# Kernel tuning notes

Hardware: AMD Instinct MI355X
Metric: run time of the kernel (lower is better)

The kernel has to match this reference:

```python
import jax, jax.numpy as jnp
import numpy as np

B, T, C, H = 4, 2048, 1024, 16
HD = C // H

def setup_inputs() -> dict:
    key = jax.random.key(0)
    ks = jax.random.split(key, 9)
    s = 1.0 / np.sqrt(C)
    return {
        'x':  jax.random.normal(ks[0], (B, T, C), jnp.float32),
        'Wq': jax.random.normal(ks[1], (C, C), jnp.float32) * s,
        'bq': jnp.zeros((C,), jnp.float32),
        'Wk': jax.random.normal(ks[2], (C, C), jnp.float32) * s,
        'bk': jnp.zeros((C,), jnp.float32),
        'Wv': jax.random.normal(ks[3], (C, C), jnp.float32) * s,
        'bv': jnp.zeros((C,), jnp.float32),
        'Wo': jax.random.normal(ks[4], (C, C), jnp.float32) * s,
        'bo': jnp.zeros((C,), jnp.float32),
    }

def reference(x, Wq, bq, Wk, bk, Wv, bv, Wo, bo):
    Bx, Tx, Cx = x.shape
    # projections (torch Linear: x @ W.T + b); split heads -> (B,H,T,HD)
    def heads(y):
        return y.reshape(Bx, Tx, H, HD).transpose(0, 2, 1, 3)
    q = heads(x @ Wq.T + bq)
    k = heads(x @ Wk.T + bk)
    v = heads(x @ Wv.T + bv)
    # NOTE: original scales by 1/sqrt(embedding_dim), not head_dim
    scale = 1.0 / jnp.sqrt(jnp.asarray(Cx, x.dtype))
    att = jnp.einsum('bhqd,bhkd->bhqk', q, k) * scale
    mask = jnp.tril(jnp.ones((Tx, Tx), dtype=bool))
    att = jnp.where(mask, att, jnp.asarray(-jnp.inf, att.dtype))
    att = jax.nn.softmax(att, axis=-1)
    y = jnp.einsum('bhqk,bhkd->bhqd', att, v)
    y = y.transpose(0, 2, 1, 3).reshape(Bx, Tx, Cx)
    return y @ Wo.T + bo
```

## Files before the change

### kernel.cpp

```cpp
#include <hip/hip_runtime.h>
#include <hip/hip_bf16.h>
#include <stdint.h>

#define NB 4
#define NT 2048
#define NC 1024
#define NH 16
#define NHD 64
#define NM (NB*NT)

typedef __attribute__((ext_vector_type(8))) __bf16 bf16x8;
typedef __attribute__((ext_vector_type(4))) float floatx4;
typedef __attribute__((ext_vector_type(8))) unsigned short ushortx8;

#define AS1(p) ((const __attribute__((address_space(1))) void*)(p))
#define AS3(p) ((__attribute__((address_space(3))) void*)(p))

__device__ __forceinline__ unsigned short f2bf(float f) {
    union { float f; unsigned int u; } v; v.f = f;
    unsigned int u = v.u;
    return (unsigned short)((u + 0x7FFFu + ((u >> 16) & 1u)) >> 16);
}
__device__ __forceinline__ unsigned int pk2(float lo, float hi) {
    union { float f; unsigned int u; } a, b; a.f = hi; b.f = lo;
    return __builtin_amdgcn_perm(a.u, b.u, 0x07060302u);
}


__global__ void cast_x_tiled(const float* __restrict__ in,
                             unsigned short* __restrict__ out, int ntiles) {
    const int wid  = (blockIdx.x * blockDim.x + threadIdx.x) >> 6;
    const int lane = threadIdx.x & 63;
    if (wid >= ntiles) return;
    const int R = wid >> 5, C = wid & 31;
    const float* src = in + ((size_t)(R*16 + (lane >> 2)))*1024 + C*32 + (lane & 3)*8;
    const floatx4 v0 = *(const floatx4*)src;
    const floatx4 v1 = *(const floatx4*)(src + 4);
    ushortx8 o;
    o[0] = f2bf(v0[0]); o[1] = f2bf(v0[1]); o[2] = f2bf(v0[2]); o[3] = f2bf(v0[3]);
    o[4] = f2bf(v1[0]); o[5] = f2bf(v1[1]); o[6] = f2bf(v1[2]); o[7] = f2bf(v1[3]);
    *(ushortx8*)&out[(size_t)wid*512 + (((lane & 3)*16 + (lane >> 2)))*8] = o;
}

__global__ void cast4_tiled(const float* __restrict__ w0, const float* __restrict__ w1,
                            const float* __restrict__ w2, const float* __restrict__ w3,
                            unsigned short* __restrict__ o0, unsigned short* __restrict__ o1,
                            unsigned short* __restrict__ o2, unsigned short* __restrict__ o3,
                            int ntiles) {
    const int wid  = (blockIdx.x * blockDim.x + threadIdx.x) >> 6;
    const int lane = threadIdx.x & 63;
    if (wid >= ntiles) return;
    const float* in; unsigned short* out;
    switch (blockIdx.y) {
        case 0: in = w0; out = o0; break;
        case 1: in = w1; out = o1; break;
        case 2: in = w2; out = o2; break;
        default: in = w3; out = o3; break;
    }
    const int R = wid >> 5, C = wid & 31;
    const float* src = in + ((size_t)(R*16 + (lane >> 2)))*1024 + C*32 + (lane & 3)*8;
    const floatx4 v0 = *(const floatx4*)src;
    const floatx4 v1 = *(const floatx4*)(src + 4);
    ushortx8 o;
    o[0] = f2bf(v0[0]); o[1] = f2bf(v0[1]); o[2] = f2bf(v0[2]); o[3] = f2bf(v0[3]);
    o[4] = f2bf(v1[0]); o[5] = f2bf(v1[1]); o[6] = f2bf(v1[2]); o[7] = f2bf(v1[3]);
    *(ushortx8*)&out[(size_t)wid*512 + (((lane & 3)*16 + (lane >> 2)))*8] = o;
}

#define TM 128
#define TN 128
#define BK 32

__device__ __forceinline__ void gemm_core(
    const unsigned short* __restrict__ A,
    const unsigned short* __restrict__ W,
    const float* __restrict__ bias,
    void* __restrict__ Out,
    unsigned short* As, unsigned short* Bs,
    int m_base, int n_base, int N_out, int K, int mode, float oscale)
{
    const int tid  = threadIdx.x;
    const int lane = tid & 63;
    const int wv   = tid >> 6;
    const int quad = lane >> 4;
    const int l16  = lane & 15;
    const int wm = (wv >> 1) * 64;
    const int wn = (wv & 1) * 64;

    floatx4 acc[4][4];
    #pragma unroll
    for (int i = 0; i < 4; ++i)
        #pragma unroll
        for (int j = 0; j < 4; ++j)
            acc[i][j] = (floatx4){0.f, 0.f, 0.f, 0.f};

    const int kTiles = K / BK;
    const int kct = K >> 5;

    const unsigned short* At = A + ((size_t)((m_base >> 4) + wv*2) * kct) * 512 + (size_t)lane*8;
    const unsigned short* Wt = W + ((size_t)((n_base >> 4) + wv*2) * kct) * 512 + (size_t)lane*8;
    const size_t rstride = (size_t)kct * 512;

    for (int kt = 0; kt < kTiles; ++kt) {
        __syncthreads();
        #pragma unroll
        for (int i = 0; i < 2; ++i) {
            __builtin_amdgcn_global_load_lds(
                AS1(At + (size_t)kt*512 + i*rstride),
                AS3(&As[(wv*2 + i)*512]), 16, 0, 0);
            __builtin_amdgcn_global_load_lds(
                AS1(Wt + (size_t)kt*512 + i*rstride),
                AS3(&Bs[(wv*2 + i)*512]), 16, 0, 0);
        }
        __syncthreads();

        bf16x8 af[4], bfr[4];
        #pragma unroll
        for (int mi = 0; mi < 4; ++mi)
            af[mi] = *(const bf16x8*)&As[((wv >> 1)*4 + mi)*512 + lane*8];
        #pragma unroll
        for (int ni = 0; ni < 4; ++ni)
            bfr[ni] = *(const bf16x8*)&Bs[((wv & 1)*4 + ni)*512 + lane*8];

        #pragma unroll
        for (int mi = 0; mi < 4; ++mi)
            #pragma unroll
            for (int ni = 0; ni < 4; ++ni)
                acc[mi][ni] = __builtin_amdgcn_mfma_f32_16x16x32_bf16(
                    af[mi], bfr[ni], acc[mi][ni], 0, 0, 0);
    }

    #pragma unroll
    for (int mi = 0; mi < 4; ++mi) {
        #pragma unroll
        for (int ni = 0; ni < 4; ++ni) {
            const int col = n_base + wn + ni*16 + l16;
            const float bv = bias[col & 1023];
            #pragma unroll
            for (int r = 0; r < 4; ++r) {
                const int row = m_base + wm + mi*16 + quad*4 + r;
                const float v = (acc[mi][ni][r] + bv) * oscale;
                if (mode == 0) {
                    ((float*)Out)[(size_t)row * N_out + col] = v;
                } else if (mode == 1) {
                    const int bb = row >> 11, t = row & (NT - 1);
                    const int h  = (col >> 6) & (NH - 1), d = col & 63;
                    const int bh = bb * NH + h;
                    const size_t idx =
                        ((size_t)((bh*128 + (t >> 4))*2 + (d >> 5)))*512
                        + (size_t)((((d >> 3) & 3)*16 + (t & 15))*8 + (d & 7));
                    ((unsigned short*)Out)[idx] = f2bf(v);
                } else {
                    const int bb = row >> 11, t = row & (NT - 1);
                    const int h  = (col >> 6) & (NH - 1), hd = col & 63;
                    const int bh = bb * NH + h;
                    const int tk = t & 31;
                    const int qv = (tk >> 2) & 3;
                    const int jv = (tk & 3) + ((tk >> 4) << 2);
                    const size_t idx =
                        ((size_t)((bh*64 + (t >> 5))*4 + (hd >> 4)))*512
                        + (size_t)((qv*16 + (hd & 15))*8 + jv);
                    ((unsigned short*)Out)[idx] = f2bf(v);
                }
            }
        }
    }
}

#define QSCALE (0.03125f * 1.44269504088896340736f)

__global__ __launch_bounds__(256) void gemm_qkv(
    const unsigned short* __restrict__ A,
    const unsigned short* __restrict__ Wq, const unsigned short* __restrict__ Wk,
    const unsigned short* __restrict__ Wv,
    const float* __restrict__ bq, const float* __restrict__ bk,
    const float* __restrict__ bv,
    unsigned short* __restrict__ Qo, unsigned short* __restrict__ Ko,
    unsigned short* __restrict__ Vo)
{
    __shared__ __align__(16) unsigned short As[TM*BK];
    __shared__ __align__(16) unsigned short Bs[TN*BK];
    const int wi = blockIdx.y >> 3;
    const int n_base = (blockIdx.y & 7) * TN;
    const unsigned short* W; const float* bias; void* Out; int mode; float osc;
    if (wi == 0)      { W = Wq; bias = bq; Out = Qo; mode = 1; osc = QSCALE; }
    else if (wi == 1) { W = Wk; bias = bk; Out = Ko; mode = 1; osc = 1.0f; }
    else              { W = Wv; bias = bv; Out = Vo; mode = 2; osc = 1.0f; }
    gemm_core(A, W, bias, Out, As, Bs, blockIdx.x * TM, n_base, NC, NC, mode, osc);
}

__global__ __launch_bounds__(256) void gemm_out(
    const unsigned short* __restrict__ A,
    const unsigned short* __restrict__ W,
    const float* __restrict__ bias,
    float* __restrict__ Out)
{
    __shared__ __align__(16) unsigned short As[TM*BK];
    __shared__ __align__(16) unsigned short Bs[TN*BK];
    gemm_core(A, W, bias, Out, As, Bs, blockIdx.x * TM, blockIdx.y * TN,
              NC, NC, 0, 1.0f);
}

__device__ __forceinline__ void attn_q32(
    const unsigned short* __restrict__ Qf,
    const unsigned short* __restrict__ Kf,
    const unsigned short* __restrict__ Vf,
    unsigned short* __restrict__ Y,
    int bh, int st, int lane)
{
    const int quad = lane >> 4, l16 = lane & 15;
    const int q0 = st * 32;
    const int b = bh >> 4, h = bh & (NH - 1);

    const size_t qbase = ((size_t)(bh*128 + st*2))*1024 + (size_t)lane*8;
    const bf16x8 qa0 = *(const bf16x8*)&Qf[qbase];
    const bf16x8 qa1 = *(const bf16x8*)&Qf[qbase + 512];
    const bf16x8 qb0 = *(const bf16x8*)&Qf[qbase + 1024];
    const bf16x8 qb1 = *(const bf16x8*)&Qf[qbase + 1536];

    const unsigned short* kp = Kf + (size_t)bh*131072 + (size_t)lane*8;
    const unsigned short* vp = Vf + (size_t)bh*131072 + (size_t)lane*8;

    floatx4 oa[4], ob[4];
    #pragma unroll
    for (int nt = 0; nt < 4; ++nt) {
        oa[nt] = (floatx4){0.f,0.f,0.f,0.f};
        ob[nt] = (floatx4){0.f,0.f,0.f,0.f};
    }
    float la = 0.f, lb = 0.f;

    const int Ffull = q0 >> 6;
    const int ntile = Ffull + 1;

    for (int f = 0; f < ntile; ++f) {
        const int j0 = f * 64;
        const bool diag = (f == Ffull);
        bf16x8 kf[4][2], vf[4][2];
        {
            const unsigned short* kt = kp + (size_t)(j0 >> 4) * 1024;
            #pragma unroll
            for (int ct = 0; ct < 4; ++ct) {
                kf[ct][0] = *(const bf16x8*)&kt[ct*1024];
                kf[ct][1] = *(const bf16x8*)&kt[ct*1024 + 512];
            }
            const unsigned short* vt = vp + (size_t)(j0 >> 5) * 2048;
            #pragma unroll
            for (int nt = 0; nt < 4; ++nt) {
                vf[nt][0] = *(const bf16x8*)&vt[nt*512];
                vf[nt][1] = *(const bf16x8*)&vt[2048 + nt*512];
            }
        }
        #pragma unroll
        for (int sub = 0; sub < 2; ++sub) {
            const bf16x8 qx0 = sub ? qb0 : qa0;
            const bf16x8 qx1 = sub ? qb1 : qa1;
            floatx4* ox = sub ? ob : oa;

            floatx4 s[4];
            __builtin_amdgcn_s_setprio(1);
            #pragma unroll
            for (int ct = 0; ct < 4; ++ct) {
                s[ct] = (floatx4){0.f,0.f,0.f,0.f};
                s[ct] = __builtin_amdgcn_mfma_f32_16x16x32_bf16(kf[ct][0], qx0, s[ct], 0,0,0);
                s[ct] = __builtin_amdgcn_mfma_f32_16x16x32_bf16(kf[ct][1], qx1, s[ct], 0,0,0);
            }
            __builtin_amdgcn_s_setprio(0);
            float p[4][4];
            float lsum = 0.f;
            if (!diag) {
                #pragma unroll
                for (int ct = 0; ct < 4; ++ct)
                    #pragma unroll
                    for (int r = 0; r < 4; ++r) {
                        p[ct][r] = __builtin_amdgcn_exp2f(s[ct][r]);
                        lsum += p[ct][r];
                    }
            } else {
                const int row = q0 + sub*16 + l16;
                #pragma unroll
                for (int ct = 0; ct < 4; ++ct)
                    #pragma unroll
                    for (int r = 0; r < 4; ++r) {
                        const int key = j0 + ct*16 + quad*4 + r;
                        p[ct][r] = (key <= row) ? __builtin_amdgcn_exp2f(s[ct][r]) : 0.f;
                        lsum += p[ct][r];
                    }
            }
            if (sub) lb += lsum; else la += lsum;

            union { bf16x8 v; unsigned int u[4]; } pf0, pf1;
            pf0.u[0] = pk2(p[0][0], p[0][1]); pf0.u[1] = pk2(p[0][2], p[0][3]);
            pf0.u[2] = pk2(p[1][0], p[1][1]); pf0.u[3] = pk2(p[1][2], p[1][3]);
            pf1.u[0] = pk2(p[2][0], p[2][1]); pf1.u[1] = pk2(p[2][2], p[2][3]);
            pf1.u[2] = pk2(p[3][0], p[3][1]); pf1.u[3] = pk2(p[3][2], p[3][3]);

            __builtin_amdgcn_s_setprio(1);
            #pragma unroll
            for (int nt = 0; nt < 4; ++nt) {
                ox[nt] = __builtin_amdgcn_mfma_f32_16x16x32_bf16(vf[nt][0], pf0.v, ox[nt], 0,0,0);
                ox[nt] = __builtin_amdgcn_mfma_f32_16x16x32_bf16(vf[nt][1], pf1.v, ox[nt], 0,0,0);
            }
            __builtin_amdgcn_s_setprio(0);
        }
    }

    la += __shfl_xor(la, 16); la += __shfl_xor(la, 32);
    lb += __shfl_xor(lb, 16); lb += __shfl_xor(lb, 32);
    const float ia = 1.0f / la, ib = 1.0f / lb;

    const size_t Rbase = (size_t)((b*NT + q0) >> 4);
    const int cg = (quad >> 1), co = (quad & 1)*4;
    #pragma unroll
    for (int nt = 0; nt < 4; ++nt) {
        const size_t base = ((Rbase*32 + h*2 + (nt >> 1))*512)
                          + (size_t)((((nt & 1)*2 + cg)*16 + l16)*8 + co);
        ushort4 wa, wb;
        wa.x = f2bf(oa[nt][0]*ia); wa.y = f2bf(oa[nt][1]*ia);
        wa.z = f2bf(oa[nt][2]*ia); wa.w = f2bf(oa[nt][3]*ia);
        wb.x = f2bf(ob[nt][0]*ib); wb.y = f2bf(ob[nt][1]*ib);
        wb.z = f2bf(ob[nt][2]*ib); wb.w = f2bf(ob[nt][3]*ib);
        *(ushort4*)&Y[base]         = wa;
        *(ushort4*)&Y[base + 16384] = wb;
    }
}

__global__ __launch_bounds__(256) void flash_attn(
    const unsigned short* __restrict__ Qf,
    const unsigned short* __restrict__ Kf,
    const unsigned short* __restrict__ Vf,
    unsigned short* __restrict__ Y)
{
    const int tid  = threadIdx.x;
    const int wave = tid >> 6;
    const int lane = tid & 63;
    const int L  = blockIdx.x;
    const int bh = (L & 7) * 8 + ((L >> 3) & 7);
    const int x  = L >> 6;
    const int w  = x * 4 + wave;
    attn_q32(Qf, Kf, Vf, Y, bh, w, lane);
    attn_q32(Qf, Kf, Vf, Y, bh, 63 - w, lane);
}

extern "C" void kernel_launch(void* const* d_in, const int* in_sizes, int n_in,
                              void* d_out, int out_size, void* d_ws, size_t ws_size,
                              hipStream_t stream) {
    const float* x  = (const float*)d_in[0];
    const float* Wq = (const float*)d_in[1];
    const float* bq = (const float*)d_in[2];
    const float* Wk = (const float*)d_in[3];
    const float* bk = (const float*)d_in[4];
    const float* Wv = (const float*)d_in[5];
    const float* bv = (const float*)d_in[6];
    const float* Wo = (const float*)d_in[7];
    const float* bo = (const float*)d_in[8];

    char* ws = (char*)d_ws;
    size_t off = 0;
    auto alloc = [&](size_t bytes) -> void* {
        void* p = ws + off;
        off += (bytes + 255) & ~(size_t)255;
        return p;
    };
    unsigned short* xb  = (unsigned short*)alloc((size_t)NM * NC * 2);
    unsigned short* Wqb = (unsigned short*)alloc((size_t)NC * NC * 2);
    unsigned short* Wkb = (unsigned short*)alloc((size_t)NC * NC * 2);
    unsigned short* Wvb = (unsigned short*)alloc((size_t)NC * NC * 2);
    unsigned short* Wob = (unsigned short*)alloc((size_t)NC * NC * 2);
    unsigned short* Qb  = (unsigned short*)alloc((size_t)NM * NC * 2);
    unsigned short* Kb  = (unsigned short*)alloc((size_t)NM * NC * 2);
    unsigned short* Vtb = (unsigned short*)alloc((size_t)NM * NC * 2);
    unsigned short* Yb  = (unsigned short*)alloc((size_t)NM * NC * 2);

    const int ntx = NM * NC / 512;
    const int ntw = NC * NC / 512;
    cast_x_tiled<<<(ntx*64 + 255)/256, 256, 0, stream>>>(x, xb, ntx);
    cast4_tiled<<<dim3((ntw*64 + 255)/256, 4), 256, 0, stream>>>(
        Wq, Wk, Wv, Wo, Wqb, Wkb, Wvb, Wob, ntw);

    gemm_qkv<<<dim3(NM / TM, 24), 256, 0, stream>>>(
        xb, Wqb, Wkb, Wvb, bq, bk, bv, Qb, Kb, Vtb);

    flash_attn<<<dim3(512), 256, 0, stream>>>(Qb, Kb, Vtb, Yb);

    gemm_out<<<dim3(NM / TM, NC / TN), 256, 0, stream>>>(Yb, Wob, bo, (float*)d_out);
}
```

Before: 241.8 us.

## Share K/V tile loads across paired query strips and template GEMM epilogues

The attention kernel now processes the two query strips of a wave (w and 63-w) together in one key loop, so each K/V tile is loaded from global memory once and used for both strips instead of being reloaded for each. The GEMM core is templated on output mode, removing runtime mode branches. For Q/K outputs it swaps the MFMA operands so each lane holds four consecutive head dims and writes them as one vectorized ushort4 store. The V epilogue also packs four values into one store. The fused attention loop holds more live registers (two sets of Q fragments and accumulators), and launch bounds now request 2 blocks per CU, which may cause spills or lower occupancy.

```diff
diff --git a/kernel.cpp b/kernel.cpp
--- a/kernel.cpp
+++ b/kernel.cpp
@@ -71,13 +71,14 @@
 #define TN 128
 #define BK 32
 
+template<int MODE>
 __device__ __forceinline__ void gemm_core(
     const unsigned short* __restrict__ A,
     const unsigned short* __restrict__ W,
     const float* __restrict__ bias,
     void* __restrict__ Out,
     unsigned short* As, unsigned short* Bs,
-    int m_base, int n_base, int N_out, int K, int mode, float oscale)
+    int m_base, int n_base, float oscale)
 {
     const int tid  = threadIdx.x;
     const int lane = tid & 63;
@@ -94,8 +95,8 @@
         for (int j = 0; j < 4; ++j)
             acc[i][j] = (floatx4){0.f, 0.f, 0.f, 0.f};
 
-    const int kTiles = K / BK;
-    const int kct = K >> 5;
+    const int kTiles = NC / BK;
+    const int kct = NC >> 5;
 
     const unsigned short* At = A + ((size_t)((m_base >> 4) + wv*2) * kct) * 512 + (size_t)lane*8;
     const unsigned short* Wt = W + ((size_t)((n_base >> 4) + wv*2) * kct) * 512 + (size_t)lane*8;
@@ -125,43 +126,64 @@
         #pragma unroll
         for (int mi = 0; mi < 4; ++mi)
             #pragma unroll
-            for (int ni = 0; ni < 4; ++ni)
-                acc[mi][ni] = __builtin_amdgcn_mfma_f32_16x16x32_bf16(
-                    af[mi], bfr[ni], acc[mi][ni], 0, 0, 0);
+            for (int ni = 0; ni < 4; ++ni) {
+                if (MODE == 1)
+                    acc[mi][ni] = __builtin_amdgcn_mfma_f32_16x16x32_bf16(
+                        bfr[ni], af[mi], acc[mi][ni], 0, 0, 0);
+                else
+                    acc[mi][ni] = __builtin_amdgcn_mfma_f32_16x16x32_bf16(
+                        af[mi], bfr[ni], acc[mi][ni], 0, 0, 0);
+            }
     }
 
     #pragma unroll
     for (int mi = 0; mi < 4; ++mi) {
         #pragma unroll
         for (int ni = 0; ni < 4; ++ni) {
-            const int col = n_base + wn + ni*16 + l16;
-            const float bv = bias[col & 1023];
-            #pragma unroll
-            for (int r = 0; r < 4; ++r) {
-                const int row = m_base + wm + mi*16 + quad*4 + r;
-                const float v = (acc[mi][ni][r] + bv) * oscale;
-                if (mode == 0) {
-                    ((float*)Out)[(size_t)row * N_out + col] = v;
-                } else if (mode == 1) {
-                    const int bb = row >> 11, t = row & (NT - 1);
-                    const int h  = (col >> 6) & (NH - 1), d = col & 63;
-                    const int bh = bb * NH + h;
-                    const size_t idx =
-                        ((size_t)((bh*128 + (t >> 4))*2 + (d >> 5)))*512
-                        + (size_t)((((d >> 3) & 3)*16 + (t & 15))*8 + (d & 7));
-                    ((unsigned short*)Out)[idx] = f2bf(v);
-                } else {
-                    const int bb = row >> 11, t = row & (NT - 1);
-                    const int h  = (col >> 6) & (NH - 1), hd = col & 63;
-                    const int bh = bb * NH + h;
-                    const int tk = t & 31;
-                    const int qv = (tk >> 2) & 3;
-                    const int jv = (tk & 3) + ((tk >> 4) << 2);
-                    const size_t idx =
-                        ((size_t)((bh*64 + (t >> 5))*4 + (hd >> 4)))*512
-                        + (size_t)((qv*16 + (hd & 15))*8 + jv);
-                    ((unsigned short*)Out)[idx] = f2bf(v);
+            if (MODE == 0) {
+                const int col = n_base + wn + ni*16 + l16;
+                const float bv = bias[col & 1023];
+                #pragma unroll
+                for (int r = 0; r < 4; ++r) {
+                    const int row = m_base + wm + mi*16 + quad*4 + r;
+                    ((float*)Out)[(size_t)row * NC + col] =
+                        (acc[mi][ni][r] + bv) * oscale;
                 }
+            } else if (MODE == 1) {
+                const int d0 = n_base + wn + ni*16 + quad*4;
+                const int t  = m_base + wm + mi*16 + l16;
+                const float4 b4 = *(const float4*)&bias[d0];
+                const int bb = t >> 11, tt = t & (NT - 1);
+                const int h  = (d0 >> 6) & (NH - 1), dd0 = d0 & 63;
+                const int bh = bb * NH + h;
+                const size_t idx0 =
+                    ((size_t)((bh*128 + (tt >> 4))*2 + (dd0 >> 5)))*512
+                    + (size_t)((((dd0 >> 3) & 3)*16 + (tt & 15))*8 + (dd0 & 7));
+                ushort4 st;
+                st.x = f2bf((acc[mi][ni][0] + b4.x) * oscale);
+                st.y = f2bf((acc[mi][ni][1] + b4.y) * oscale);
+                st.z = f2bf((acc[mi][ni][2] + b4.z) * oscale);
+                st.w = f2bf((acc[mi][ni][3] + b4.w) * oscale);
+                *(ushort4*)&((unsigned short*)Out)[idx0] = st;
+            } else {
+                const int col = n_base + wn + ni*16 + l16;
+                const float bv = bias[col & 1023];
+                const int row0 = m_base + wm + mi*16 + quad*4;
+                const int bb = row0 >> 11, t0 = row0 & (NT - 1);
+                const int h  = (col >> 6) & (NH - 1), hd = col & 63;
+                const int bh = bb * NH + h;
+                const int tk0 = t0 & 31;
+                const int qv  = (tk0 >> 2) & 3;
+                const int jv0 = (tk0 >> 4) << 2;
+                const size_t idx0 =
+                    ((size_t)((bh*64 + (t0 >> 5))*4 + (hd >> 4)))*512
+                    + (size_t)((qv*16 + (hd & 15))*8 + jv0);
+                ushort4 st;
+                st.x = f2bf((acc[mi][ni][0] + bv) * oscale);
+                st.y = f2bf((acc[mi][ni][1] + bv) * oscale);
+                st.z = f2bf((acc[mi][ni][2] + bv) * oscale);
+                st.w = f2bf((acc[mi][ni][3] + bv) * oscale);
+                *(ushort4*)&((unsigned short*)Out)[idx0] = st;
             }
         }
     }
@@ -182,11 +204,13 @@
     __shared__ __align__(16) unsigned short Bs[TN*BK];
     const int wi = blockIdx.y >> 3;
     const int n_base = (blockIdx.y & 7) * TN;
-    const unsigned short* W; const float* bias; void* Out; int mode; float osc;
-    if (wi == 0)      { W = Wq; bias = bq; Out = Qo; mode = 1; osc = QSCALE; }
-    else if (wi == 1) { W = Wk; bias = bk; Out = Ko; mode = 1; osc = 1.0f; }
-    else              { W = Wv; bias = bv; Out = Vo; mode = 2; osc = 1.0f; }
-    gemm_core(A, W, bias, Out, As, Bs, blockIdx.x * TM, n_base, NC, NC, mode, osc);
+    const int m_base = blockIdx.x * TM;
+    if (wi == 0)
+        gemm_core<1>(A, Wq, bq, Qo, As, Bs, m_base, n_base, QSCALE);
+    else if (wi == 1)
+        gemm_core<1>(A, Wk, bk, Ko, As, Bs, m_base, n_base, 1.0f);
+    else
+        gemm_core<2>(A, Wv, bv, Vo, As, Bs, m_base, n_base, 1.0f);
 }
 
 __global__ __launch_bounds__(256) void gemm_out(
@@ -197,117 +221,76 @@
 {
     __shared__ __align__(16) unsigned short As[TM*BK];
     __shared__ __align__(16) unsigned short Bs[TN*BK];
-    gemm_core(A, W, bias, Out, As, Bs, blockIdx.x * TM, blockIdx.y * TN,
-              NC, NC, 0, 1.0f);
-}
-
-__device__ __forceinline__ void attn_q32(
-    const unsigned short* __restrict__ Qf,
-    const unsigned short* __restrict__ Kf,
-    const unsigned short* __restrict__ Vf,
-    unsigned short* __restrict__ Y,
-    int bh, int st, int lane)
-{
-    const int quad = lane >> 4, l16 = lane & 15;
-    const int q0 = st * 32;
-    const int b = bh >> 4, h = bh & (NH - 1);
-
-    const size_t qbase = ((size_t)(bh*128 + st*2))*1024 + (size_t)lane*8;
-    const bf16x8 qa0 = *(const bf16x8*)&Qf[qbase];
-    const bf16x8 qa1 = *(const bf16x8*)&Qf[qbase + 512];
-    const bf16x8 qb0 = *(const bf16x8*)&Qf[qbase + 1024];
-    const bf16x8 qb1 = *(const bf16x8*)&Qf[qbase + 1536];
-
-    const unsigned short* kp = Kf + (size_t)bh*131072 + (size_t)lane*8;
-    const unsigned short* vp = Vf + (size_t)bh*131072 + (size_t)lane*8;
-
-    floatx4 oa[4], ob[4];
+    gemm_core<0>(A, W, bias, Out, As, Bs, blockIdx.x * TM, blockIdx.y * TN, 1.0f);
+}
+
+__device__ __forceinline__ void attn_tile(
+    const bf16x8 kf[4][2], const bf16x8 vf[4][2],
+    const bf16x8 q[4], floatx4 o[2][4], float l[2],
+    bool diag, int q0, int j0, int quad, int l16)
+{
     #pragma unroll
-    for (int nt = 0; nt < 4; ++nt) {
-        oa[nt] = (floatx4){0.f,0.f,0.f,0.f};
-        ob[nt] = (floatx4){0.f,0.f,0.f,0.f};
-    }
-    float la = 0.f, lb = 0.f;
-
-    const int Ffull = q0 >> 6;
-    const int ntile = Ffull + 1;
-
-    for (int f = 0; f < ntile; ++f) {
-        const int j0 = f * 64;
-        const bool diag = (f == Ffull);
-        bf16x8 kf[4][2], vf[4][2];
-        {
-            const unsigned short* kt = kp + (size_t)(j0 >> 4) * 1024;
+    for (int sub = 0; sub < 2; ++sub) {
+        const bf16x8 qx0 = q[sub*2];
+        const bf16x8 qx1 = q[sub*2 + 1];
+
+        floatx4 s[4];
+        __builtin_amdgcn_s_setprio(1);
+        #pragma unroll
+        for (int ct = 0; ct < 4; ++ct) {
+            s[ct] = (floatx4){0.f,0.f,0.f,0.f};
+            s[ct] = __builtin_amdgcn_mfma_f32_16x16x32_bf16(kf[ct][0], qx0, s[ct], 0,0,0);
+            s[ct] = __builtin_amdgcn_mfma_f32_16x16x32_bf16(kf[ct][1], qx1, s[ct], 0,0,0);
+        }
+        __builtin_amdgcn_s_setprio(0);
+
+        float p[4][4];
+        float lsum = 0.f;
+        if (!diag) {
             #pragma unroll
-            for (int ct = 0; ct < 4; ++ct) {
-                kf[ct][0] = *(const bf16x8*)&kt[ct*1024];
-                kf[ct][1] = *(const bf16x8*)&kt[ct*1024 + 512];
-            }
-            const unsigned short* vt = vp + (size_t)(j0 >> 5) * 2048;
+            for (int ct = 0; ct < 4; ++ct)
+                #pragma unroll
+                for (int r = 0; r < 4; ++r) {
+                    p[ct][r] = __builtin_amdgcn_exp2f(s[ct][r]);
+                    lsum += p[ct][r];
+                }
+        } else {
+            const int row = q0 + sub*16 + l16;
             #pragma unroll
-            for (int nt = 0; nt < 4; ++nt) {
-                vf[nt][0] = *(const bf16x8*)&vt[nt*512];
-                vf[nt][1] = *(const bf16x8*)&vt[2048 + nt*512];
-            }
-        }
-        #pragma unroll
-        for (int sub = 0; sub < 2; ++sub) {
-            const bf16x8 qx0 = sub ? qb0 : qa0;
-            const bf16x8 qx1 = sub ? qb1 : qa1;
-            floatx4* ox = sub ? ob : oa;
-
-            floatx4 s[4];
-            __builtin_amdgcn_s_setprio(1);
-            #pragma unroll
-            for (int ct = 0; ct < 4; ++ct) {
-                s[ct] = (floatx4){0.f,0.f,0.f,0.f};
-                s[ct] = __builtin_amdgcn_mfma_f32_16x16x32_bf16(kf[ct][0], qx0, s[ct], 0,0,0);
-                s[ct] = __builtin_amdgcn_mfma_f32_16x16x32_bf16(kf[ct][1], qx1, s[ct], 0,0,0);
-            }
-            __builtin_amdgcn_s_setprio(0);
-            float p[4][4];
-            float lsum = 0.f;
-            if (!diag) {
+            for (int ct = 0; ct < 4; ++ct)
                 #pragma unroll
-                for (int ct = 0; ct < 4; ++ct)
-                    #pragma unroll
-                    for (int r = 0; r < 4; ++r) {
-                        p[ct][r] = __builtin_amdgcn_exp2f(s[ct][r]);
-                        lsum += p[ct][r];
-                    }
-            } else {
-                const int row = q0 + sub*16 + l16;
-                #pragma unroll
-                for (int ct = 0; ct < 4; ++ct)
-                    #pragma unroll
-                    for (int r = 0; r < 4; ++r) {
-                        const int key = j0 + ct*16 + quad*4 + r;
-                        p[ct][r] = (key <= row) ? __builtin_amdgcn_exp2f(s[ct][r]) : 0.f;
-                        lsum += p[ct][r];
-                    }
-            }
-            if (sub) lb += lsum; else la += lsum;
-
-            union { bf16x8 v; unsigned int u[4]; } pf0, pf1;
-            pf0.u[0] = pk2(p[0][0], p[0][1]); pf0.u[1] = pk2(p[0][2], p[0][3]);
-            pf0.u[2] = pk2(p[1][0], p[1][1]); pf0.u[3] = pk2(p[1][2], p[1][3]);
-            pf1.u[0] = pk2(p[2][0], p[2][1]); pf1.u[1] = pk2(p[2][2], p[2][3]);
-            pf1.u[2] = pk2(p[3][0], p[3][1]); pf1.u[3] = pk2(p[3][2], p[3][3]);
-
-            __builtin_amdgcn_s_setprio(1);
-            #pragma unroll
-            for (int nt = 0; nt < 4; ++nt) {
-                ox[nt] = __builtin_amdgcn_mfma_f32_16x16x32_bf16(vf[nt][0], pf0.v, ox[nt], 0,0,0);
-                ox[nt] = __builtin_amdgcn_mfma_f32_16x16x32_bf16(vf[nt][1], pf1.v, ox[nt], 0,0,0);
-            }
-            __builtin_amdgcn_s_setprio(0);
-        }
-    }
-
+                for (int r = 0; r < 4; ++r) {
+                    const int key = j0 + ct*16 + quad*4 + r;
+                    p[ct][r] = (key <= row) ? __builtin_amdgcn_exp2f(s[ct][r]) : 0.f;
+                    lsum += p[ct][r];
+                }
+        }
+        l[sub] += lsum;
+
+        union { bf16x8 v; unsigned int u[4]; } pf0, pf1;
+        pf0.u[0] = pk2(p[0][0], p[0][1]); pf0.u[1] = pk2(p[0][2], p[0][3]);
+        pf0.u[2] = pk2(p[1][0], p[1][1]); pf0.u[3] = pk2(p[1][2], p[1][3]);
+        pf1.u[0] = pk2(p[2][0], p[2][1]); pf1.u[1] = pk2(p[2][2], p[2][3]);
+        pf1.u[2] = pk2(p[3][0], p[3][1]); pf1.u[3] = pk2(p[3][2], p[3][3]);
+
+        __builtin_amdgcn_s_setprio(1);
+        #pragma unroll
+        for (int nt = 0; nt < 4; ++nt) {
+            o[sub][nt] = __builtin_amdgcn_mfma_f32_16x16x32_bf16(vf[nt][0], pf0.v, o[sub][nt], 0,0,0);
+            o[sub][nt] = __builtin_amdgcn_mfma_f32_16x16x32_bf16(vf[nt][1], pf1.v, o[sub][nt], 0,0,0);
+        }
+        __builtin_amdgcn_s_setprio(0);
+    }
+}
+
+__device__ __forceinline__ void attn_store(
+    unsigned short* __restrict__ Y, const floatx4 o[2][4], const float l[2],
+    int q0, int b, int h, int quad, int l16)
+{
+    float la = l[0], lb = l[1];
     la += __shfl_xor(la, 16); la += __shfl_xor(la, 32);
     lb += __shfl_xor(lb, 16); lb += __shfl_xor(lb, 32);
     const float ia = 1.0f / la, ib = 1.0f / lb;
-
     const size_t Rbase = (size_t)((b*NT + q0) >> 4);
     const int cg = (quad >> 1), co = (quad & 1)*4;
     #pragma unroll
@@ -315,16 +298,78 @@
         const size_t base = ((Rbase*32 + h*2 + (nt >> 1))*512)
                           + (size_t)((((nt & 1)*2 + cg)*16 + l16)*8 + co);
         ushort4 wa, wb;
-        wa.x = f2bf(oa[nt][0]*ia); wa.y = f2bf(oa[nt][1]*ia);
-        wa.z = f2bf(oa[nt][2]*ia); wa.w = f2bf(oa[nt][3]*ia);
-        wb.x = f2bf(ob[nt][0]*ib); wb.y = f2bf(ob[nt][1]*ib);
-        wb.z = f2bf(ob[nt][2]*ib); wb.w = f2bf(ob[nt][3]*ib);
+        wa.x = f2bf(o[0][nt][0]*ia); wa.y = f2bf(o[0][nt][1]*ia);
+        wa.z = f2bf(o[0][nt][2]*ia); wa.w = f2bf(o[0][nt][3]*ia);
+        wb.x = f2bf(o[1][nt][0]*ib); wb.y = f2bf(o[1][nt][1]*ib);
+        wb.z = f2bf(o[1][nt][2]*ib); wb.w = f2bf(o[1][nt][3]*ib);
         *(ushort4*)&Y[base]         = wa;
         *(ushort4*)&Y[base + 16384] = wb;
     }
 }
 
-__global__ __launch_bounds__(256) void flash_attn(
+__device__ __forceinline__ void attn_pair(
+    const unsigned short* __restrict__ Qf,
+    const unsigned short* __restrict__ Kf,
+    const unsigned short* __restrict__ Vf,
+    unsigned short* __restrict__ Y,
+    int bh, int stA, int stB, int lane)
+{
+    const int quad = lane >> 4, l16 = lane & 15;
+    const int b = bh >> 4, h = bh & (NH - 1);
+    const int q0A = stA * 32, q0B = stB * 32;
+    const int FA = q0A >> 6, FB = q0B >> 6;
+
+    const size_t qbA = ((size_t)(bh*128 + stA*2))*1024 + (size_t)lane*8;
+    const size_t qbB = ((size_t)(bh*128 + stB*2))*1024 + (size_t)lane*8;
+    bf16x8 qA[4], qB[4];
+    qA[0] = *(const bf16x8*)&Qf[qbA];
+    qA[1] = *(const bf16x8*)&Qf[qbA + 512];
+    qA[2] = *(const bf16x8*)&Qf[qbA + 1024];
+    qA[3] = *(const bf16x8*)&Qf[qbA + 1536];
+    qB[0] = *(const bf16x8*)&Qf[qbB];
+    qB[1] = *(const bf16x8*)&Qf[qbB + 512];
+    qB[2] = *(const bf16x8*)&Qf[qbB + 1024];
+    qB[3] = *(const bf16x8*)&Qf[qbB + 1536];
+
+    const unsigned short* kp = Kf + (size_t)bh*131072 + (size_t)lane*8;
+    const unsigned short* vp = Vf + (size_t)bh*131072 + (size_t)lane*8;
+
+    floatx4 oA[2][4], oB[2][4];
+    float lA[2] = {0.f, 0.f}, lB[2] = {0.f, 0.f};
+    #pragma unroll
+    for (int s2 = 0; s2 < 2; ++s2)
+        #pragma unroll
+        for (int nt = 0; nt < 4; ++nt) {
+            oA[s2][nt] = (floatx4){0.f,0.f,0.f,0.f};
+            oB[s2][nt] = (floatx4){0.f,0.f,0.f,0.f};
+        }
+
+    for (int f = 0; f <= FB; ++f) {
+        const int j0 = f * 64;
+        bf16x8 kf[4][2], vf[4][2];
+        const unsigned short* kt = kp + (size_t)f * 4096;
+        #pragma unroll
+        for (int ct = 0; ct < 4; ++ct) {
+            kf[ct][0] = *(const bf16x8*)&kt[ct*1024];
+            kf[ct][1] = *(const bf16x8*)&kt[ct*1024 + 512];
+        }
+        const unsigned short* vt = vp + (size_t)f * 4096;
+        #pragma unroll
+        for (int nt = 0; nt < 4; ++nt) {
+            vf[nt][0] = *(const bf16x8*)&vt[nt*512];
+            vf[nt][1] = *(const bf16x8*)&vt[2048 + nt*512];
+        }
+
+        if (f <= FA)
+            attn_tile(kf, vf, qA, oA, lA, f == FA, q0A, j0, quad, l16);
+        attn_tile(kf, vf, qB, oB, lB, f == FB, q0B, j0, quad, l16);
+    }
+
+    attn_store(Y, oA, lA, q0A, b, h, quad, l16);
+    attn_store(Y, oB, lB, q0B, b, h, quad, l16);
+}
+
+__global__ __launch_bounds__(256, 2) void flash_attn(
     const unsigned short* __restrict__ Qf,
     const unsigned short* __restrict__ Kf,
     const unsigned short* __restrict__ Vf,
@@ -337,8 +382,7 @@
     const int bh = (L & 7) * 8 + ((L >> 3) & 7);
     const int x  = L >> 6;
     const int w  = x * 4 + wave;
-    attn_q32(Qf, Kf, Vf, Y, bh, w, lane);
-    attn_q32(Qf, Kf, Vf, Y, bh, 63 - w, lane);
+    attn_pair(Qf, Kf, Vf, Y, bh, w, 63 - w, lane);
 }
 
 extern "C" void kernel_launch(void* const* d_in, const int* in_sizes, int n_in,
```

New measurement: 233.9 us. 1.03x faster.
